# Performance work log

Hardware: AMD Instinct MI355X
Metric: run time of the kernel (lower is better)

Reference implementation:

```python
import math
import jax, jax.numpy as jnp
import numpy as np

SAMPLE_RATIO = 0.25
K_NN = 5


def grid_index(loc_orig, H, W):
    # loc in [-1,1] -> nearest grid cell index (row-major)
    loc = jnp.clip(loc_orig, -1.0, 1.0) * 0.5 + 0.5
    ix = jnp.clip(jnp.round(loc[..., 0] * (W - 1)).astype(jnp.int32), 0, W - 1)
    iy = jnp.clip(jnp.round(loc[..., 1] * (H - 1)).astype(jnp.int32), 0, H - 1)
    return iy * W + ix  # [B, N0]


def token2map(x, loc_orig, idx_agg, H, W):
    # scatter token features (replicated to original points) into HxW grid, cell-average
    B, N, C = x.shape
    N0 = idx_agg.shape[1]
    idx_hw = grid_index(loc_orig, H, W)
    off = jnp.arange(B, dtype=jnp.int32)[:, None]
    idx_hw_flat = (idx_hw + off * (H * W)).reshape(-1)
    value = jnp.ones((B * N0,), x.dtype)
    all_w = jax.ops.segment_sum(value, idx_hw_flat, num_segments=B * H * W) + 1e-6
    value = value / all_w[idx_hw_flat]
    x_src = jnp.take_along_axis(x, idx_agg[..., None], axis=1).reshape(B * N0, C)
    x_map = jax.ops.segment_sum(x_src * value[:, None], idx_hw_flat, num_segments=B * H * W)
    return x_map.reshape(B, H, W, C).transpose(0, 3, 1, 2)  # [B,C,H,W]


def map2token(x_map, N, loc_orig, idx_agg, agg_weight):
    # gather grid features back to tokens, weighted by per-token-normalized agg_weight
    B, C, H, W = x_map.shape
    N0 = idx_agg.shape[1]
    idx_hw = grid_index(loc_orig, H, W)
    off = jnp.arange(B, dtype=jnp.int32)[:, None]
    idx_tok_flat = (idx_agg + off * N).reshape(-1)
    idx_hw_flat = (idx_hw + off * (H * W)).reshape(-1)
    value = agg_weight.reshape(-1).astype(x_map.dtype)
    all_w = jax.ops.segment_sum(value, idx_tok_flat, num_segments=B * N) + 1e-6
    value = value / all_w[idx_tok_flat]
    feat = x_map.transpose(0, 2, 3, 1).reshape(B * H * W, C)[idx_hw_flat]
    out = jax.ops.segment_sum(feat * value[:, None], idx_tok_flat, num_segments=B * N)
    return out.reshape(B, N, C)


def cluster_dpc_knn(x, Ns, k):
    # DPC-KNN clustering (no_grad in original -> stop_gradient)
    B, N, C = x.shape
    x = jax.lax.stop_gradient(x)
    x2 = jnp.sum(x * x, axis=-1)
    d2 = x2[:, :, None] + x2[:, None, :] - 2.0 * jnp.einsum('bic,bjc->bij', x, x)
    dist = jnp.sqrt(jnp.maximum(d2, 0.0)) / jnp.sqrt(jnp.asarray(C, x.dtype))
    dist_nearest = -jax.lax.top_k(-dist, k)[0]                 # k smallest dists (incl self)
    density = jnp.exp(-jnp.mean(dist_nearest ** 2, axis=-1))    # [B,N]
    # deterministic tiny tie-break noise (original uses torch.rand*1e-6)
    density = density + jax.random.uniform(jax.random.key(42), density.shape, density.dtype) * 1e-6
    mask = (density[:, None, :] > density[:, :, None]).astype(x.dtype)
    dist_max = jnp.max(dist.reshape(B, -1), axis=-1)[:, None, None]
    dist_ind = jnp.min(dist * mask + dist_max * (1.0 - mask), axis=-1)
    score = dist_ind * density
    index_down = jax.lax.top_k(score, Ns)[1]                    # [B,Ns] cluster centers
    dist_c = jnp.take_along_axis(dist, index_down[:, :, None], axis=1)  # [B,Ns,N]
    idx_cluster = jnp.argmin(dist_c, axis=1).astype(jnp.int32)  # [B,N]
    # centers belong to their own cluster
    flat = (index_down + jnp.arange(B)[:, None] * N).reshape(-1)
    own = jnp.tile(jnp.arange(Ns, dtype=jnp.int32), B)
    idx_cluster = idx_cluster.reshape(-1).at[flat].set(own).reshape(B, N)
    return idx_cluster


def merge_tokens(x, idx_cluster, Ns, weight, idx_agg):
    # weighted average of tokens per cluster; propagate mapping/weights to original points
    B, N, C = x.shape
    idx = (idx_cluster + jnp.arange(B, dtype=jnp.int32)[:, None] * Ns).reshape(-1)
    w = weight.reshape(-1)
    all_w = jax.ops.segment_sum(w, idx, num_segments=B * Ns) + 1e-6
    nw = w / all_w[idx]
    x_merged = jax.ops.segment_sum(x.reshape(B * N, C) * nw[:, None], idx,
                                   num_segments=B * Ns).reshape(B, Ns, C)
    norm_weight = nw.reshape(B, N, 1)
    idx_agg_new = jnp.take_along_axis(idx_cluster, idx_agg, axis=1)          # [B,N0]
    weight_t = jnp.take_along_axis(norm_weight, idx_agg[..., None], axis=1)  # [B,N0,1]
    return x_merged, idx_agg_new, weight_t


def ctm_forward(x, loc_orig, idx_agg, agg_weight, conv_w, conv_b, skip_w, ln_g, ln_b,
                conf_w, conf_b, H, W):
    B, N, C = x.shape
    x_map = token2map(x, loc_orig, idx_agg, H, W)
    x_map = jax.lax.conv_general_dilated(
        x_map, conv_w, window_strides=(2, 2), padding=((1, 1), (1, 1)),
        dimension_numbers=('NCHW', 'OIHW', 'NCHW')) + conv_b[None, :, None, None]
    xt = map2token(x_map, N, loc_orig, idx_agg, agg_weight) + x @ skip_w.T
    mu = jnp.mean(xt, axis=-1, keepdims=True)
    var = jnp.mean((xt - mu) ** 2, axis=-1, keepdims=True)
    xt = (xt - mu) / jnp.sqrt(var + 1e-5) * ln_g + ln_b
    conf = xt @ conf_w.T + conf_b          # [B,N,1]
    weight = jnp.exp(conf)
    Ns = max(math.ceil(N * SAMPLE_RATIO), 1)
    idx_cluster = cluster_dpc_knn(xt, Ns, K_NN)
    x_down, idx_agg_down, weight_t = merge_tokens(xt, idx_cluster, Ns, weight, idx_agg)
    agg_weight_down = agg_weight * weight_t
    agg_weight_down = agg_weight_down / jnp.max(agg_weight_down, axis=1, keepdims=True)
    # down_block is identity in this reference
    return x_down, idx_agg_down, agg_weight_down


def setup_inputs() -> dict:
    key = jax.random.key(0)
    ks = jax.random.split(key, 10)
    B, N, C, C2, H, W = 4, 3136, 64, 128, 56, 56
    return {
        'x': jax.random.normal(ks[0], (B, N, C), jnp.float32),
        'loc_orig': jax.random.normal(ks[1], (B, N, 2), jnp.float32),
        'idx_agg': jax.random.randint(ks[2], (B, N), 0, N),
        'agg_weight': jax.random.uniform(ks[3], (B, N, 1), jnp.float32, 0.1, 1.0),
        'conv_w': jax.random.normal(ks[4], (C2, C, 3, 3), jnp.float32) * 0.02,
        'conv_b': jnp.zeros((C2,), jnp.float32),
        'skip_w': jax.random.normal(ks[5], (C2, C), jnp.float32) * 0.02,
        'ln_g': jnp.ones((C2,), jnp.float32),
        'ln_b': jnp.zeros((C2,), jnp.float32),
        'conf_w': jax.random.normal(ks[6], (1, C2), jnp.float32) * 0.02,
        'conf_b': jnp.zeros((1,), jnp.float32),
        'H': 56,
        'W': 56,
    }


def reference(x, loc_orig, idx_agg, agg_weight, conv_w, conv_b, skip_w, ln_g, ln_b,
              conf_w, conf_b, H, W):
    return ctm_forward(x, loc_orig, idx_agg, agg_weight, conv_w, conv_b, skip_w,
                       ln_g, ln_b, conf_w, conf_b, H, W)
```

## Files before the change

### kernel.cpp

```cpp
#include <hip/hip_runtime.h>
#include <math.h>
#include <float.h>

#define Bq   4
#define Nq   3136
#define Cq   64
#define C2q  128
#define Hq   56
#define Wq   56
#define HWq  (Hq*Wq)
#define HOq  28
#define WOq  28
#define HWOq (HOq*WOq)
#define NSq  784
#define KNN  5
#define BNq  (Bq*Nq)

#define T64   64
#define KC    32
#define NIT64 (Nq/T64)
#define NT_C  ((NSq+T64-1)/T64)
#define NSPL  8
#define NSPA  2
#define LDP   34

__device__ __constant__ int c_spl[NSPL + 1]  = {0, 7, 13, 19, 25, 31, 37, 43, 49};
__device__ __constant__ int c_spla[NSPA + 1] = {0, 7, 13};

typedef unsigned int   u32;
typedef unsigned long long u64;
typedef __attribute__((ext_vector_type(4))) double d64x4;

static __device__ __forceinline__ void atomicMaxPosD(double* p, double v) {
    atomicMax((u64*)p, (u64)__double_as_longlong(v));
}
static __device__ __forceinline__ int clampTok(int t) {
    return min(max(t, 0), Nq - 1);
}

static __device__ __forceinline__ void ins5(double* a, double v) {
    if (v < a[KNN - 1]) {
        a[KNN - 1] = v;
        #pragma unroll
        for (int m = KNN - 1; m > 0; m--)
            if (a[m] < a[m - 1]) { double t = a[m]; a[m] = a[m - 1]; a[m - 1] = t; }
    }
}
static __device__ __forceinline__ void cex(double& a, double& b) {
    double lo = fmin(a, b), hi = fmax(a, b); a = lo; b = hi;
}
static __device__ __forceinline__ void merge5(double* a, const double* p) {
    double t0 = fmin(a[0], p[4]);
    double t1 = fmin(a[1], p[3]);
    double t2 = fmin(a[2], p[2]);
    double t3 = fmin(a[3], p[1]);
    double t4 = fmin(a[4], p[0]);
    cex(t0, t1); cex(t1, t2); cex(t2, t3); cex(t3, t4);
    cex(t0, t1); cex(t1, t2); cex(t2, t3);
    cex(t0, t1); cex(t1, t2);
    cex(t0, t1);
    a[0] = t0; a[1] = t1; a[2] = t2; a[3] = t3; a[4] = t4;
}

static __device__ __forceinline__ int mfma_mode_probe(int l4, int l15) {
    d64x4 p;
    #pragma unroll
    for (int v = 0; v < 4; v++) p[v] = 0.0;
    double a1 = (l4 == 0) ? (double)(16 * l15) : 0.0;
    double b1 = (l4 == 0) ? 1.0 : 0.0;
    p = __builtin_amdgcn_mfma_f64_16x16x4f64(a1, b1, p, 0, 0, 0);
    double a2 = (l4 == 0) ? 1.0 : 0.0;
    double b2 = (l4 == 0) ? (double)l15 : 0.0;
    p = __builtin_amdgcn_mfma_f64_16x16x4f64(a2, b2, p, 0, 0, 0);
    bool ok0 = true, ok1 = true;
    #pragma unroll
    for (int v = 0; v < 4; v++) {
        ok0 = ok0 && (p[v] == (double)(16 * (4 * l4 + v) + l15));
        ok1 = ok1 && (p[v] == (double)(16 * (l4 + 4 * v) + l15));
    }
    return __all(ok0) ? 0 : (__all(ok1) ? 1 : 2);
}

static __device__ __forceinline__ u32 rotl32(u32 x, int d) { return (x << d) | (x >> (32 - d)); }
static __device__ __forceinline__ float tf_uniform(int t) {
    const u32 k0 = 0u, k1 = 42u;
    const u32 ks2 = k0 ^ k1 ^ 0x1BD11BDAu;
    u32 ks[3] = { k0, k1, ks2 };
    bool lo = (t < 6272);
    u32 cx0 = lo ? (u32)t : (u32)(t - 6272);
    u32 cx1 = lo ? (u32)(t + 6272) : (u32)t;
    u32 x0 = cx0 + ks[0];
// ... 70 lines not shown
              const float* __restrict__ bias, double* xmap28T) {
    __shared__ double sIn[2][9][Cq];
    int blk = blockIdx.x;
    int b  = blk & (Bq - 1);
    int cp = blk >> 2;
    int tid = threadIdx.x;
    int co = tid & (C2q - 1);
    int cl = tid >> 7;
    const double* xb = xmap56T + (size_t)b * HWq * Cq;
    for (int idx = tid; idx < 2 * 9 * Cq; idx += 256) {
        int cell_l = idx / (9 * Cq);
        int rem = idx - cell_l * (9 * Cq);
        int tap = rem >> 6;
        int ci  = rem & 63;
        int cell = 2 * cp + cell_l;
        int ox = cell % WOq, oy = cell / WOq;
        int ky = tap / 3, kx = tap - ky * 3;
        int iy = 2 * oy + ky - 1, ix = 2 * ox + kx - 1;
        double v = 0.0;
        if (iy >= 0 && iy < Hq && ix >= 0 && ix < Wq)
            v = xb[(size_t)(iy * Wq + ix) * Cq + ci];
        sIn[cell_l][tap][ci] = v;
    }
    __syncthreads();
    double acc = (double)bias[co];
    for (int ci = 0; ci < Cq; ci++) {
        #pragma unroll
        for (int tap = 0; tap < 9; tap++)
            acc += sIn[cl][tap][ci] * (double)wT[(size_t)(ci * 9 + tap) * C2q + co];
    }
    int cell = 2 * cp + cl;
    xmap28T[((size_t)b * HWOq + cell) * C2q + co] = acc;
}

__global__ void ctm_m2t(const double* __restrict__ xmap28T, const float* __restrict__ aggw,
                        const int* __restrict__ idx_agg, const int* __restrict__ cell28,
                        const double* __restrict__ allwtok, double* xt) {
    int id = blockIdx.x * blockDim.x + threadIdx.x;
    if (id >= BNq * C2q) return;
    int t = id / C2q, c = id - t * C2q;
    int b = t / Nq;
    int tok = clampTok(idx_agg[t]);
    double v = (double)aggw[t] / (allwtok[b * Nq + tok] + 1e-6);
    double f = xmap28T[((size_t)b * HWOq + cell28[t]) * C2q + c];
    atomicAdd(&xt[(size_t)(b * Nq + tok) * C2q + c], f * v);
}

__global__ __launch_bounds__(C2q)
void ctm_finalize(double* xt, const float* __restrict__ x, const float* __restrict__ skipw,
                  const float* __restrict__ lng, const float* __restrict__ lnb,
                  const float* __restrict__ confw, const float* __restrict__ confb,
                  double* x2o, double* weightv) {
    int bn = blockIdx.x; int c = threadIdx.x;
    double* row = xt + (size_t)bn * C2q;
    const float* xr = x + (size_t)bn * Cq;
    double acc = row[c];
    const float* sw = skipw + c * Cq;
    #pragma unroll 16
    for (int k = 0; k < Cq; k++) acc += (double)xr[k] * (double)sw[k];
    __shared__ double red[C2q];
    __shared__ double stat[2];
    red[c] = acc; __syncthreads();
    for (int off = C2q / 2; off > 0; off >>= 1) { if (c < off) red[c] += red[c + off]; __syncthreads(); }
    if (c == 0) stat[0] = red[0] * (1.0 / C2q);
    __syncthreads();
    double mu = stat[0];
    double d = acc - mu;
    red[c] = d * d; __syncthreads();
    for (int off = C2q / 2; off > 0; off >>= 1) { if (c < off) red[c] += red[c + off]; __syncthreads(); }
    if (c == 0) stat[1] = red[0] * (1.0 / C2q);
    __syncthreads();
    double var = stat[1];
    double v = d / sqrt(var + 1e-5) * (double)lng[c] + (double)lnb[c];
    row[c] = v;
    red[c] = v * v; __syncthreads();
    for (int off = C2q / 2; off > 0; off >>= 1) { if (c < off) red[c] += red[c + off]; __syncthreads(); }
    if (c == 0) x2o[bn] = red[0];
    __syncthreads();
    red[c] = v * (double)confw[c]; __syncthreads();
    for (int off = C2q / 2; off > 0; off >>= 1) { if (c < off) red[c] += red[c + off]; __syncthreads(); }
    if (c == 0) weightv[bn] = exp(red[0] + (double)confb[0]);
}


__global__ __launch_bounds__(256, 2)
void ctm_pass1(const double* __restrict__ xt, const double* __restrict__ x2,
               double* pbest, double* pmax) {
    __shared__ double sBB[2][T64][LDP];
    __shared__ double sx2j[2][T64];
    int blk = blockIdx.x;
    int b  = blk & (Bq - 1);
    int s  = (blk >> 2) & (NSPL - 1);
    int it = blk >> 5;
    int tid = threadIdx.x;
    const double* xtb = xt + (size_t)b * Nq * C2q;
    const double* x2b = x2 + (size_t)b * Nq;
    int i0 = it * T64;
    int jt_beg = c_spl[s], jt_end = c_spl[s + 1];

    int wv = tid >> 6, ln = tid & 63;
    int l15 = ln & 15, l4 = ln >> 4;
    int mode = mfma_mode_probe(l4, l15);

    if (mode < 2) {
        int rw[4];
        #pragma unroll
        for (int v = 0; v < 4; v++) rw[v] = (mode == 0) ? (4 * l4 + v) : (l4 + 4 * v);
        int rbase = i0 + wv * 16;
        double a_reg[4][8];
        const double* arow = xtb + (size_t)(i0 + wv * 16 + l15) * C2q + l4;
        #pragma unroll
        for (int kc = 0; kc < 4; kc++)
            #pragma unroll
            for (int st = 0; st < 8; st++)
                a_reg[kc][st] = arow[kc * KC + 4 * st];
        double x2i[4];
        #pragma unroll
        for (int v = 0; v < 4; v++) x2i[v] = x2b[rbase + rw[v]];
        double best[4][KNN]; double mx[4];
        #pragma unroll
        for (int v = 0; v < 4; v++) {
            mx[v] = -DBL_MAX;
            #pragma unroll
            for (int k = 0; k < KNN; k++) best[v][k] = DBL_MAX;
        }
        {
            int j0 = jt_beg * T64;
            #pragma unroll
            for (int w = 0; w < 4; w++) {
                int idx = tid + w * 256; int r = idx >> 4, c = (idx & 15) * 2;
                *(double2*)&sBB[0][r][c] = *(const double2*)&xtb[(size_t)(j0 + r) * C2q + c];
            }
            if (tid < T64) sx2j[0][tid] = x2b[j0 + tid];
        }
        __syncthreads();
        int q = 0;
        for (int jt = jt_beg; jt < jt_end; jt++) {
            int j0 = jt * T64;
            d64x4 acc[4];
            #pragma unroll
            for (int bc = 0; bc < 4; bc++)
                #pragma unroll
                for (int v = 0; v < 4; v++) acc[bc][v] = 0.0;
            #pragma unroll
            for (int kc = 0; kc < 4; kc++) {
                const int cb = kc & 1, nb = cb ^ 1, nkc = (kc + 1) & 3;
                const bool lastk = (kc == 3);
                bool hn = !lastk || (jt + 1 < jt_end);
                int nj0 = lastk ? j0 + T64 : j0;
                double2 sreg[4]; double xr = 0.0;
                if (hn) {
                    #pragma unroll
                    for (int w = 0; w < 4; w++) {
                        int idx = tid + w * 256; int r = idx >> 4, c = (idx & 15) * 2;
                        sreg[w] = *(const double2*)&xtb[(size_t)(nj0 + r) * C2q + nkc * KC + c];
                    }
                    if (lastk && tid < T64) xr = x2b[nj0 + tid];
                }
                #pragma unroll
                for (int st = 0; st < 8; st++) {
                    double av = a_reg[kc][st];
                    #pragma unroll
                    for (int bc = 0; bc < 4; bc++) {
                        double bv = sBB[cb][bc * 16 + l15][4 * st + l4];
                        acc[bc] = __builtin_amdgcn_mfma_f64_16x16x4f64(av, bv, acc[bc], 0, 0, 0);
                    }
                }
                if (hn) {
                    #pragma unroll
                    for (int w = 0; w < 4; w++) {
                        int idx = tid + w * 256; int r = idx >> 4, c = (idx & 15) * 2;
                        *(double2*)&sBB[nb][r][c] = sreg[w];
                    }
                    if (lastk && tid < T64) sx2j[q ^ 1][tid] = xr;
                }
                __syncthreads();
            }
            #pragma unroll
            for (int bc = 0; bc < 4; bc++) {
                double xj = sx2j[q][bc * 16 + l15];
                #pragma unroll
                for (int v = 0; v < 4; v++) {
                    double d2 = x2i[v] + xj - 2.0 * acc[bc][v];
                    mx[v] = fmax(mx[v], d2);
                    ins5(best[v], d2);
                }
            }
            q ^= 1;
        }
        for (int m = 1; m <= 8; m <<= 1) {
            #pragma unroll
            for (int v = 0; v < 4; v++) {
                double p[KNN];
                #pragma unroll
                for (int k = 0; k < KNN; k++) p[k] = __shfl_xor(best[v][k], m);
                mx[v] = fmax(mx[v], __shfl_xor(mx[v], m));
                merge5(best[v], p);
            }
        }
        if (l15 == 0) {
            #pragma unroll
            for (int v = 0; v < 4; v++) {
                int gi = b * Nq + rbase + rw[v];
                size_t base = ((size_t)s * BNq + gi) * KNN;
                #pragma unroll
                for (int k = 0; k < KNN; k++) pbest[base + k] = best[v][k];
                pmax[(size_t)s * BNq + gi] = mx[v];
            }
        }
    } else {
        double (*sA)[LDP] = sBB[0];
        double (*sB)[LDP] = sBB[1];
        int tx = tid & 15, ty = tid >> 4;
        double x2i[4];
        #pragma unroll
        for (int r = 0; r < 4; r++) x2i[r] = x2b[i0 + ty + 16 * r];
        double best[4][KNN]; double mx[4];
        #pragma unroll
        for (int r = 0; r < 4; r++) {
            mx[r] = -DBL_MAX;
            #pragma unroll
            for (int k = 0; k < KNN; k++) best[r][k] = DBL_MAX;
        }
        for (int jt = jt_beg; jt < jt_end; jt++) {
            int j0 = jt * T64;
            double acc[4][4];
            #pragma unroll
            for (int r = 0; r < 4; r++)
                #pragma unroll
                for (int q = 0; q < 4; q++) acc[r][q] = 0.0;
            for (int kc = 0; kc < 4; kc++) {
                __syncthreads();
                #pragma unroll
                for (int idx = tid; idx < T64 * KC / 2; idx += 256) {
                    int r = idx >> 4, c = (idx & 15) * 2;
                    *(double2*)&sA[r][c] = *(const double2*)&xtb[(size_t)(i0 + r) * C2q + kc * KC + c];
                    *(double2*)&sB[r][c] = *(const double2*)&xtb[(size_t)(j0 + r) * C2q + kc * KC + c];
                }
                if (kc == 0 && tid < T64) sx2j[0][tid] = x2b[j0 + tid];
                __syncthreads();
                #pragma unroll 4
                for (int cc = 0; cc < KC; cc += 2) {
                    double2 xi[4], xj[4];
                    #pragma unroll
                    for (int r = 0; r < 4; r++) xi[r] = *(const double2*)&sA[ty + 16 * r][cc];
                    #pragma unroll
                    for (int q = 0; q < 4; q++) xj[q] = *(const double2*)&sB[tx + 16 * q][cc];
                    #pragma unroll
                    for (int r = 0; r < 4; r++)
                        #pragma unroll
                        for (int q = 0; q < 4; q++) acc[r][q] += xi[r].x * xj[q].x;
                    #pragma unroll
                    for (int r = 0; r < 4; r++)
                        #pragma unroll
                        for (int q = 0; q < 4; q++) acc[r][q] += xi[r].y * xj[q].y;
                }
            }
            #pragma unroll
            for (int r = 0; r < 4; r++)
                #pragma unroll
                for (int q = 0; q < 4; q++) {
                    double d2 = x2i[r] + sx2j[0][tx + 16 * q] - 2.0 * acc[r][q];
                    mx[r] = fmax(mx[r], d2);
                    ins5(best[r], d2);
                }
        }
        for (int m = 1; m <= 8; m <<= 1) {
            #pragma unroll
            for (int r = 0; r < 4; r++) {
                double p[KNN];
                #pragma unroll
                for (int k = 0; k < KNN; k++) p[k] = __shfl_xor(best[r][k], m);
                mx[r] = fmax(mx[r], __shfl_xor(mx[r], m));
                merge5(best[r], p);
            }
        }
        if (tx == 0) {
            #pragma unroll
            for (int r = 0; r < 4; r++) {
                int gi = b * Nq + i0 + ty + 16 * r;
                size_t base = ((size_t)s * BNq + gi) * KNN;
                #pragma unroll
                for (int k = 0; k < KNN; k++) pbest[base + k] = best[r][k];
                pmax[(size_t)s * BNq + gi] = mx[r];
            }
        }
    }
}

__global__ void ctm_merge1(const double* __restrict__ pbest, const double* __restrict__ pmax,
                           double* density, double* maxd2) {
    int t = blockIdx.x * blockDim.x + threadIdx.x;
    if (t >= BNq) return;
    double a[KNN];
    #pragma unroll
    for (int k = 0; k < KNN; k++) a[k] = pbest[(size_t)t * KNN + k];
    double mxv = pmax[t];
    #pragma unroll
    for (int s = 1; s < NSPL; s++) {
        double p[KNN];
        #pragma unroll
        for (int k = 0; k < KNN; k++) p[k] = pbest[((size_t)s * BNq + t) * KNN + k];
        merge5(a, p);
        mxv = fmax(mxv, pmax[(size_t)s * BNq + t]);
    }
    double sum = 0.0;
    #pragma unroll
    for (int k = 0; k < KNN; k++) sum += fmax(a[k], 0.0);
    density[t] = exp(-sum / (double)(C2q * KNN)) + (double)(tf_uniform(t) * 1e-6f);
    atomicMaxPosD(&maxd2[t / Nq], mxv);
}

__global__ __launch_bounds__(256, 2)
void ctm_pass2(const double* __restrict__ xt, const double* __restrict__ x2,
               const double* __restrict__ density, double* pmin) {
    __shared__ double sBB[2][T64][LDP];
    __shared__ double sx2j[2][T64];
    __shared__ double sdj[2][T64];
    int blk = blockIdx.x;
    int b  = blk & (Bq - 1);
    int s  = (blk >> 2) & (NSPL - 1);
    int it = blk >> 5;
    int tid = threadIdx.x;
    const double* xtb = xt + (size_t)b * Nq * C2q;
    const double* x2b = x2 + (size_t)b * Nq;
    const double* db  = density + (size_t)b * Nq;
    int i0 = it * T64;
    int jt_beg = c_spl[s], jt_end = c_spl[s + 1];

    int wv = tid >> 6, ln = tid & 63;
    int l15 = ln & 15, l4 = ln >> 4;
    int mode = mfma_mode_probe(l4, l15);

    if (mode < 2) {
        int rw[4];
        #pragma unroll
        for (int v = 0; v < 4; v++) rw[v] = (mode == 0) ? (4 * l4 + v) : (l4 + 4 * v);
        int rbase = i0 + wv * 16;
        double a_reg[4][8];
        const double* arow = xtb + (size_t)(i0 + wv * 16 + l15) * C2q + l4;
        #pragma unroll
        for (int kc = 0; kc < 4; kc++)
            #pragma unroll
            for (int st = 0; st < 8; st++)
                a_reg[kc][st] = arow[kc * KC + 4 * st];
        double x2i[4], di[4], mn[4];
        #pragma unroll
        for (int v = 0; v < 4; v++) {
            x2i[v] = x2b[rbase + rw[v]];
            di[v]  = db[rbase + rw[v]];
            mn[v]  = DBL_MAX;
        }
        {
            int j0 = jt_beg * T64;
            #pragma unroll
            for (int w = 0; w < 4; w++) {
                int idx = tid + w * 256; int r = idx >> 4, c = (idx & 15) * 2;
                *(double2*)&sBB[0][r][c] = *(const double2*)&xtb[(size_t)(j0 + r) * C2q + c];
            }
            if (tid < T64) { sx2j[0][tid] = x2b[j0 + tid]; sdj[0][tid] = db[j0 + tid]; }
        }
        __syncthreads();
        int q = 0;
        for (int jt = jt_beg; jt < jt_end; jt++) {
            int j0 = jt * T64;
            d64x4 acc[4];
            #pragma unroll
            for (int bc = 0; bc < 4; bc++)
                #pragma unroll
                for (int v = 0; v < 4; v++) acc[bc][v] = 0.0;
            #pragma unroll
            for (int kc = 0; kc < 4; kc++) {
                const int cb = kc & 1, nb = cb ^ 1, nkc = (kc + 1) & 3;
                const bool lastk = (kc == 3);
                bool hn = !lastk || (jt + 1 < jt_end);
                int nj0 = lastk ? j0 + T64 : j0;
                double2 sreg[4]; double xr = 0.0, dr = 0.0;
                if (hn) {
                    #pragma unroll
                    for (int w = 0; w < 4; w++) {
                        int idx = tid + w * 256; int r = idx >> 4, c = (idx & 15) * 2;
                        sreg[w] = *(const double2*)&xtb[(size_t)(nj0 + r) * C2q + nkc * KC + c];
                    }
                    if (lastk && tid < T64) { xr = x2b[nj0 + tid]; dr = db[nj0 + tid]; }
                }
                #pragma unroll
                for (int st = 0; st < 8; st++) {
                    double av = a_reg[kc][st];
                    #pragma unroll
                    for (int bc = 0; bc < 4; bc++) {
                        double bv = sBB[cb][bc * 16 + l15][4 * st + l4];
                        acc[bc] = __builtin_amdgcn_mfma_f64_16x16x4f64(av, bv, acc[bc], 0, 0, 0);
                    }
                }
                if (hn) {
                    #pragma unroll
                    for (int w = 0; w < 4; w++) {
                        int idx = tid + w * 256; int r = idx >> 4, c = (idx & 15) * 2;
                        *(double2*)&sBB[nb][r][c] = sreg[w];
                    }
                    if (lastk && tid < T64) { sx2j[q ^ 1][tid] = xr; sdj[q ^ 1][tid] = dr; }
                }
                __syncthreads();
            }
            #pragma unroll
            for (int bc = 0; bc < 4; bc++) {
                double xj = sx2j[q][bc * 16 + l15];
                double dj = sdj[q][bc * 16 + l15];
                #pragma unroll
                for (int v = 0; v < 4; v++) {
                    double d2 = x2i[v] + xj - 2.0 * acc[bc][v];
                    if (dj > di[v]) mn[v] = fmin(mn[v], d2);
                }
            }
            q ^= 1;
        }
        for (int m = 1; m <= 8; m <<= 1) {
            #pragma unroll
            for (int v = 0; v < 4; v++) mn[v] = fmin(mn[v], __shfl_xor(mn[v], m));
        }
        if (l15 == 0) {
            #pragma unroll
            for (int v = 0; v < 4; v++) {
                int gi = b * Nq + rbase + rw[v];
                pmin[(size_t)s * BNq + gi] = mn[v];
            }
        }
    } else {
        double (*sA)[LDP] = sBB[0];
        double (*sB)[LDP] = sBB[1];
        int tx = tid & 15, ty = tid >> 4;
        double x2i[4], di[4], mn[4];
        #pragma unroll
        for (int r = 0; r < 4; r++) {
            x2i[r] = x2b[i0 + ty + 16 * r];
            di[r]  = db[i0 + ty + 16 * r];
            mn[r]  = DBL_MAX;
        }
        for (int jt = jt_beg; jt < jt_end; jt++) {
            int j0 = jt * T64;
            double acc[4][4];
            #pragma unroll
            for (int r = 0; r < 4; r++)
                #pragma unroll
                for (int q = 0; q < 4; q++) acc[r][q] = 0.0;
            for (int kc = 0; kc < 4; kc++) {
                __syncthreads();
                #pragma unroll
                for (int idx = tid; idx < T64 * KC / 2; idx += 256) {
                    int r = idx >> 4, c = (idx & 15) * 2;
                    *(double2*)&sA[r][c] = *(const double2*)&xtb[(size_t)(i0 + r) * C2q + kc * KC + c];
                    *(double2*)&sB[r][c] = *(const double2*)&xtb[(size_t)(j0 + r) * C2q + kc * KC + c];
                }
                if (kc == 0 && tid < T64) { sx2j[0][tid] = x2b[j0 + tid]; sdj[0][tid] = db[j0 + tid]; }
                __syncthreads();
                #pragma unroll 4
                for (int cc = 0; cc < KC; cc += 2) {
                    double2 xi[4], xj[4];
                    #pragma unroll
                    for (int r = 0; r < 4; r++) xi[r] = *(const double2*)&sA[ty + 16 * r][cc];
                    #pragma unroll
                    for (int q = 0; q < 4; q++) xj[q] = *(const double2*)&sB[tx + 16 * q][cc];
                    #pragma unroll
                    for (int r = 0; r < 4; r++)
                        #pragma unroll
                        for (int q = 0; q < 4; q++) acc[r][q] += xi[r].x * xj[q].x;
                    #pragma unroll
                    for (int r = 0; r < 4; r++)
                        #pragma unroll
                        for (int q = 0; q < 4; q++) acc[r][q] += xi[r].y * xj[q].y;
                }
            }
            #pragma unroll
            for (int r = 0; r < 4; r++)
                #pragma unroll
                for (int q = 0; q < 4; q++) {
                    double d2 = x2i[r] + sx2j[0][tx + 16 * q] - 2.0 * acc[r][q];
                    if (sdj[0][tx + 16 * q] > di[r]) mn[r] = fmin(mn[r], d2);
                }
        }
        for (int m = 1; m <= 8; m <<= 1) {
            #pragma unroll
            for (int r = 0; r < 4; r++) mn[r] = fmin(mn[r], __shfl_xor(mn[r], m));
        }
        if (tx == 0) {
            #pragma unroll
            for (int r = 0; r < 4; r++) {
                int gi = b * Nq + i0 + ty + 16 * r;
                pmin[(size_t)s * BNq + gi] = mn[r];
            }
        }
    }
}

__global__ void ctm_merge2(const double* __restrict__ pmin, const double* __restrict__ maxd2,
                           const double* __restrict__ density, double* score) {
    int t = blockIdx.x * blockDim.x + threadIdx.x;
    if (t >= BNq) return;
    int b = t / Nq;
    double m = pmin[t];
    #pragma unroll
    for (int s = 1; s < NSPL; s++) m = fmin(m, pmin[(size_t)s * BNq + t]);
    double mm = fmin(maxd2[b], m);
    score[t] = sqrt(fmax(mm, 0.0)) / sqrt((double)C2q) * density[t];
}

__global__ __launch_bounds__(1024)
void ctm_sort(const double* __restrict__ score, int* index_down) {
    __shared__ double s[4096];
    __shared__ int   si[4096];
    int b = blockIdx.x, tid = threadIdx.x;
    for (int i = tid; i < 4096; i += 1024) {
        if (i < Nq) {
            double v = score[b * Nq + i];
            s[i] = isnan(v) ? -DBL_MAX : v;
            si[i] = i;
        } else { s[i] = -DBL_MAX; si[i] = 0x7fffffff; }
    }
    __syncthreads();
    for (int k = 2; k <= 4096; k <<= 1) {
        for (int j = k >> 1; j > 0; j >>= 1) {
            for (int i = tid; i < 4096; i += 1024) {
                int ixj = i ^ j;
                if (ixj > i) {
                    double s1 = s[i], s2 = s[ixj];
                    int i1 = si[i], i2 = si[ixj];
                    bool before_ij = (s1 > s2) || (s1 == s2 && i1 < i2);
                    bool before_ji = (s2 > s1) || (s2 == s1 && i2 < i1);
                    bool doswap = ((i & k) == 0) ? before_ji : before_ij;
                    if (doswap) { s[i] = s2; s[ixj] = s1; si[i] = i2; si[ixj] = i1; }
                }
            }
            __syncthreads();
        }
    }
    for (int t = tid; t < NSq; t += 1024) {
        int v = si[t];
        index_down[b * NSq + t] = ((unsigned)v < (unsigned)Nq) ? v : 0;
    }
}

__global__ __launch_bounds__(256, 2)
void ctm_assign(const double* __restrict__ xt, const double* __restrict__ x2,
                const int* __restrict__ index_down, double* pbd, int* pbs) {
    __shared__ double sBB[2][T64][LDP];
    __shared__ double sx2c[T64];
    __shared__ int    sidx[T64];
    int blk = blockIdx.x;
    int b  = blk & (Bq - 1);
    int s  = (blk >> 2) & (NSPA - 1);
    int it = blk >> 3;
    int tid = threadIdx.x;
    const double* xtb = xt + (size_t)b * Nq * C2q;
    const double* x2b = x2 + (size_t)b * Nq;
    int i0 = it * T64;
    int jt_beg = c_spla[s], jt_end = c_spla[s + 1];

// ... 218 lines not shown
}

__global__ void ctm_out2(const double* __restrict__ awd, const double* __restrict__ maxawd, float* out2) {
    int t = blockIdx.x * blockDim.x + threadIdx.x;
    if (t >= BNq) return;
    int b = t / Nq;
    out2[t] = (float)(awd[t] / maxawd[b]);
}

extern "C" void kernel_launch(void* const* d_in, const int* in_sizes, int n_in,
                              void* d_out, int out_size, void* d_ws, size_t ws_size,
                              hipStream_t stream) {
    const float* x     = (const float*)d_in[0];
    const float* loc   = (const float*)d_in[1];
    const int*   idxag = (const int*)  d_in[2];
    const float* aggw  = (const float*)d_in[3];
    const float* convw = (const float*)d_in[4];
    const float* convb = (const float*)d_in[5];
    const float* skipw = (const float*)d_in[6];
    const float* lng   = (const float*)d_in[7];
    const float* lnb   = (const float*)d_in[8];
    const float* confw = (const float*)d_in[9];
    const float* confb = (const float*)d_in[10];
    (void)in_sizes; (void)n_in;

    char* w = (char*)d_ws;
    size_t off = 0;
    auto alloc = [&](size_t bytes) -> void* {
        void* p = w + off; off = (off + bytes + 255) & ~(size_t)255; return p;
    };

    int*    cnt56   = (int*)   alloc((size_t)BNq * 4);
    double* allwtok = (double*)alloc((size_t)BNq * 8);
    double* xt      = (double*)alloc((size_t)BNq * C2q * 8);
    double* arena   = (double*)alloc((size_t)Bq * HWq * Cq * 8);
    double* allwc   = (double*)alloc((size_t)Bq * NSq * 8);
    double* maxawd  = (double*)alloc((size_t)Bq * 8);
    double* maxd2   = (double*)alloc((size_t)Bq * 8);
    size_t zero_bytes = off;
    int*    cell56   = (int*)   alloc((size_t)BNq * 4);
    int*    cell28   = (int*)   alloc((size_t)BNq * 4);
    double* xmap28T  = (double*)alloc((size_t)Bq * HWOq * C2q * 8);
    float*  wT       = (float*) alloc((size_t)C2q * Cq * 9 * 4);
    double* x2       = (double*)alloc((size_t)BNq * 8);
    double* density  = (double*)alloc((size_t)BNq * 8);
    double* score    = (double*)alloc((size_t)BNq * 8);
    int*    indexdn  = (int*)   alloc((size_t)Bq * NSq * 4);
    int*    idxclu   = (int*)   alloc((size_t)BNq * 4);
    double* nw       = (double*)alloc((size_t)BNq * 8);
    double* weightv  = (double*)alloc((size_t)BNq * 8);
    double* awd      = (double*)alloc((size_t)BNq * 8);
    double* pbest    = (double*)alloc((size_t)NSPL * BNq * KNN * 8);
    double* pmax     = (double*)alloc((size_t)NSPL * BNq * 8);
    double* pmin     = (double*)alloc((size_t)NSPL * BNq * 8);
    double* pbd      = (double*)alloc((size_t)NSPA * BNq * 8);
    int*    pbs      = (int*)   alloc((size_t)NSPA * BNq * 4);
    size_t required = off;

    const int tb = 256;
    float* out = (float*)d_out;

    if (ws_size < required) {
        ctm_fallback<<<(out_size + tb - 1) / tb, tb, 0, stream>>>(out, out_size);
        return;
    }

    double* xmap56T = arena;
    double* xmerged = arena;

    hipMemsetAsync(d_ws, 0, zero_bytes, stream);

    ctm_prep<<<(BNq + tb - 1) / tb, tb, 0, stream>>>(loc, idxag, aggw, cell56, cell28, cnt56, allwtok);
    ctm_wt<<<((C2q * Cq * 9) + tb - 1) / tb, tb, 0, stream>>>(convw, wT);
    ctm_t2m<<<((BNq * Cq) + tb - 1) / tb, tb, 0, stream>>>(x, idxag, cell56, cnt56, xmap56T);
    ctm_conv<<<Bq * (HWOq / 2), 256, 0, stream>>>(xmap56T, wT, convb, xmap28T);
    ctm_m2t<<<((BNq * C2q) + tb - 1) / tb, tb, 0, stream>>>(xmap28T, aggw, idxag, cell28, allwtok, xt);
    ctm_finalize<<<BNq, C2q, 0, stream>>>(xt, x, skipw, lng, lnb, confw, confb, x2, weightv);
    ctm_pass1<<<Bq * NSPL * NIT64, 256, 0, stream>>>(xt, x2, pbest, pmax);
    ctm_merge1<<<(BNq + tb - 1) / tb, tb, 0, stream>>>(pbest, pmax, density, maxd2);
    ctm_pass2<<<Bq * NSPL * NIT64, 256, 0, stream>>>(xt, x2, density, pmin);
    ctm_merge2<<<(BNq + tb - 1) / tb, tb, 0, stream>>>(pmin, maxd2, density, score);
    ctm_sort<<<Bq, 1024, 0, stream>>>(score, indexdn);
    ctm_assign<<<Bq * NSPA * NIT64, 256, 0, stream>>>(xt, x2, indexdn, pbd, pbs);
    ctm_merge3<<<(BNq + tb - 1) / tb, tb, 0, stream>>>(pbd, pbs, idxclu);
    ctm_override<<<((Bq * NSq) + tb - 1) / tb, tb, 0, stream>>>(indexdn, idxclu);
    ctm_zeromerged<<<((Bq * NSq * C2q) + tb - 1) / tb, tb, 0, stream>>>(xmerged);
    ctm_merge_w<<<(BNq + tb - 1) / tb, tb, 0, stream>>>(idxclu, weightv, allwc);
    ctm_merge_x<<<((BNq * C2q) + tb - 1) / tb, tb, 0, stream>>>(idxclu, weightv, allwc, xt, nw, xmerged);

    ctm_out0<<<((Bq * NSq * C2q) + tb - 1) / tb, tb, 0, stream>>>(xmerged, out);
    ctm_out12<<<(BNq + tb - 1) / tb, tb, 0, stream>>>(idxag, idxclu, nw, aggw,
                                                      out + (size_t)Bq * NSq * C2q, awd, maxawd);
    ctm_out2<<<(BNq + tb - 1) / tb, tb, 0, stream>>>(awd, maxawd,
                                                     out + (size_t)Bq * NSq * C2q + BNq);
}
```

Before: 1.237 ms.

## Cache pairwise distances in pass1 and replace pass2 GEMM with streaming min scan

New measurement: 1.237 ms. About the same (+0.0%).

```diff
diff --git a/kernel.cpp b/kernel.cpp
--- a/kernel.cpp
+++ b/kernel.cpp
@@ -213,40 +213,48 @@
                   const float* __restrict__ confw, const float* __restrict__ confb,
                   double* x2o, double* weightv) {
     int bn = blockIdx.x; int c = threadIdx.x;
+    int lane = c & 63, w = c >> 6;
     double* row = xt + (size_t)bn * C2q;
     const float* xr = x + (size_t)bn * Cq;
     double acc = row[c];
     const float* sw = skipw + c * Cq;
     #pragma unroll 16
     for (int k = 0; k < Cq; k++) acc += (double)xr[k] * (double)sw[k];
-    __shared__ double red[C2q];
-    __shared__ double stat[2];
-    red[c] = acc; __syncthreads();
-    for (int off = C2q / 2; off > 0; off >>= 1) { if (c < off) red[c] += red[c + off]; __syncthreads(); }
-    if (c == 0) stat[0] = red[0] * (1.0 / C2q);
+    __shared__ double slot[4][2];
+    double s = acc;
+    #pragma unroll
+    for (int m = 1; m <= 32; m <<= 1) s += __shfl_xor(s, m);
+    if (lane == 0) slot[0][w] = s;
     __syncthreads();
-    double mu = stat[0];
+    double mu = (slot[0][0] + slot[0][1]) * (1.0 / C2q);
     double d = acc - mu;
-    red[c] = d * d; __syncthreads();
-    for (int off = C2q / 2; off > 0; off >>= 1) { if (c < off) red[c] += red[c + off]; __syncthreads(); }
-    if (c == 0) stat[1] = red[0] * (1.0 / C2q);
+    s = d * d;
+    #pragma unroll
+    for (int m = 1; m <= 32; m <<= 1) s += __shfl_xor(s, m);
+    if (lane == 0) slot[1][w] = s;
     __syncthreads();
-    double var = stat[1];
+    double var = (slot[1][0] + slot[1][1]) * (1.0 / C2q);
     double v = d / sqrt(var + 1e-5) * (double)lng[c] + (double)lnb[c];
     row[c] = v;
-    red[c] = v * v; __syncthreads();
-    for (int off = C2q / 2; off > 0; off >>= 1) { if (c < off) red[c] += red[c + off]; __syncthreads(); }
-    if (c == 0) x2o[bn] = red[0];
+    s = v * v;
+    #pragma unroll
+    for (int m = 1; m <= 32; m <<= 1) s += __shfl_xor(s, m);
+    if (lane == 0) slot[2][w] = s;
+    double s2 = v * (double)confw[c];
+    #pragma unroll
+    for (int m = 1; m <= 32; m <<= 1) s2 += __shfl_xor(s2, m);
+    if (lane == 0) slot[3][w] = s2;
     __syncthreads();
-    red[c] = v * (double)confw[c]; __syncthreads();
-    for (int off = C2q / 2; off > 0; off >>= 1) { if (c < off) red[c] += red[c + off]; __syncthreads(); }
-    if (c == 0) weightv[bn] = exp(red[0] + (double)confb[0]);
+    if (c == 0) {
+        x2o[bn] = slot[2][0] + slot[2][1];
+        weightv[bn] = exp(slot[3][0] + slot[3][1] + (double)confb[0]);
+    }
 }
 
 
 __global__ __launch_bounds__(256, 2)
 void ctm_pass1(const double* __restrict__ xt, const double* __restrict__ x2,
-               double* pbest, double* pmax) {
+               double* pbest, double* pmax, double* d2buf, int dostore) {
     __shared__ double sBB[2][T64][LDP];
     __shared__ double sx2j[2][T64];
     int blk = blockIdx.x;
@@ -343,6 +351,8 @@
                 #pragma unroll
                 for (int v = 0; v < 4; v++) {
                     double d2 = x2i[v] + xj - 2.0 * acc[bc][v];
+                    if (dostore)
+                        d2buf[(size_t)(b * Nq + rbase + rw[v]) * Nq + (j0 + bc * 16 + l15)] = d2;
                     mx[v] = fmax(mx[v], d2);
                     ins5(best[v], d2);
                 }
@@ -422,6 +432,8 @@
                 #pragma unroll
                 for (int q = 0; q < 4; q++) {
                     double d2 = x2i[r] + sx2j[0][tx + 16 * q] - 2.0 * acc[r][q];
+                    if (dostore)
+                        d2buf[(size_t)(b * Nq + i0 + ty + 16 * r) * Nq + (j0 + tx + 16 * q)] = d2;
                     mx[r] = fmax(mx[r], d2);
                     ins5(best[r], d2);
                 }
@@ -470,6 +482,36 @@
     for (int k = 0; k < KNN; k++) sum += fmax(a[k], 0.0);
     density[t] = exp(-sum / (double)(C2q * KNN)) + (double)(tf_uniform(t) * 1e-6f);
     atomicMaxPosD(&maxd2[t / Nq], mxv);
+}
+
+__global__ __launch_bounds__(256)
+void ctm_pass2s(const double* __restrict__ d2buf, const double* __restrict__ density,
+                double* pmin2) {
+    int gid = blockIdx.x * 4 + (threadIdx.x >> 6);
+    int lane = threadIdx.x & 63;
+    if (gid >= BNq) return;
+    int b = gid / Nq;
+    int i = gid - b * Nq;
+    const double* dr = d2buf + (size_t)gid * Nq;
+    const double* db = density + (size_t)b * Nq;
+    double di = db[i];
+    double mn = DBL_MAX;
+    for (int j = lane; j < Nq; j += 64) {
+        double d2 = dr[j];
+        if (db[j] > di) mn = fmin(mn, d2);
+    }
+    #pragma unroll
+    for (int m = 1; m <= 32; m <<= 1) mn = fmin(mn, __shfl_xor(mn, m));
+    if (lane == 0) pmin2[gid] = mn;
+}
+
+__global__ void ctm_merge2s(const double* __restrict__ pmin2, const double* __restrict__ maxd2,
+                            const double* __restrict__ density, double* score) {
+    int t = blockIdx.x * blockDim.x + threadIdx.x;
+    if (t >= BNq) return;
+    int b = t / Nq;
+    double mm = fmin(maxd2[b], pmin2[t]);
+    score[t] = sqrt(fmax(mm, 0.0)) / sqrt((double)C2q) * density[t];
 }
 
 __global__ __launch_bounds__(256, 2)
@@ -992,6 +1034,8 @@
     double* pbd      = (double*)alloc((size_t)NSPA * BNq * 8);
     int*    pbs      = (int*)   alloc((size_t)NSPA * BNq * 4);
     size_t required = off;
+    double* d2buf    = (double*)alloc((size_t)BNq * Nq * 8);
+    size_t required_fast = off;
 
     const int tb = 256;
     float* out = (float*)d_out;
@@ -1000,6 +1044,7 @@
         ctm_fallback<<<(out_size + tb - 1) / tb, tb, 0, stream>>>(out, out_size);
         return;
     }
+    const bool fast = (ws_size >= required_fast);
 
     double* xmap56T = arena;
     double* xmerged = arena;
@@ -1012,10 +1057,15 @@
     ctm_conv<<<Bq * (HWOq / 2), 256, 0, stream>>>(xmap56T, wT, convb, xmap28T);
     ctm_m2t<<<((BNq * C2q) + tb - 1) / tb, tb, 0, stream>>>(xmap28T, aggw, idxag, cell28, allwtok, xt);
     ctm_finalize<<<BNq, C2q, 0, stream>>>(xt, x, skipw, lng, lnb, confw, confb, x2, weightv);
-    ctm_pass1<<<Bq * NSPL * NIT64, 256, 0, stream>>>(xt, x2, pbest, pmax);
+    ctm_pass1<<<Bq * NSPL * NIT64, 256, 0, stream>>>(xt, x2, pbest, pmax, d2buf, fast ? 1 : 0);
     ctm_merge1<<<(BNq + tb - 1) / tb, tb, 0, stream>>>(pbest, pmax, density, maxd2);
-    ctm_pass2<<<Bq * NSPL * NIT64, 256, 0, stream>>>(xt, x2, density, pmin);
-    ctm_merge2<<<(BNq + tb - 1) / tb, tb, 0, stream>>>(pmin, maxd2, density, score);
+    if (fast) {
+        ctm_pass2s<<<(BNq + 3) / 4, 256, 0, stream>>>(d2buf, density, pmin);
+        ctm_merge2s<<<(BNq + tb - 1) / tb, tb, 0, stream>>>(pmin, maxd2, density, score);
+    } else {
+        ctm_pass2<<<Bq * NSPL * NIT64, 256, 0, stream>>>(xt, x2, density, pmin);
+        ctm_merge2<<<(BNq + tb - 1) / tb, tb, 0, stream>>>(pmin, maxd2, density, score);
+    }
     ctm_sort<<<Bq, 1024, 0, stream>>>(score, indexdn);
     ctm_assign<<<Bq * NSPA * NIT64, 256, 0, stream>>>(xt, x2, indexdn, pbd, pbs);
     ctm_merge3<<<(BNq + tb - 1) / tb, tb, 0, stream>>>(pbd, pbs, idxclu);
```

## Sort tokens by density and compute only lower-triangular tiles for parent distance

Applied to the files above, without the earlier changes.

Result: no change. 1.218 ms (-1.5%).

```diff
diff --git a/kernel.cpp b/kernel.cpp
--- a/kernel.cpp
+++ b/kernel.cpp
@@ -19,7 +19,7 @@
 #define T64   64
 #define KC    32
 #define NIT64 (Nq/T64)
-#define NT_C  ((NSq+T64-1)/T64)
+#define NPAIR (NIT64*(NIT64+1)/2)
 #define NSPL  8
 #define NSPA  2
 #define LDP   34
@@ -37,6 +37,16 @@
 static __device__ __forceinline__ int clampTok(int t) {
     return min(max(t, 0), Nq - 1);
 }
+
+static __device__ __forceinline__ u64 encD(double d) {
+    u64 u = (u64)__double_as_longlong(d);
+    return (u >> 63) ? ~u : (u | 0x8000000000000000ULL);
+}
+static __device__ __forceinline__ double decD(u64 u) {
+    u64 o = (u >> 63) ? (u ^ 0x8000000000000000ULL) : ~u;
+    return __longlong_as_double((long long)o);
+}
+#define ENC_DBL_MAX 0xFFEFFFFFFFFFFFFFULL
 
 static __device__ __forceinline__ void ins5(double* a, double v) {
     if (v < a[KNN - 1]) {
@@ -213,34 +223,42 @@
                   const float* __restrict__ confw, const float* __restrict__ confb,
                   double* x2o, double* weightv) {
     int bn = blockIdx.x; int c = threadIdx.x;
+    int lane = c & 63, w = c >> 6;
     double* row = xt + (size_t)bn * C2q;
     const float* xr = x + (size_t)bn * Cq;
     double acc = row[c];
     const float* sw = skipw + c * Cq;
     #pragma unroll 16
     for (int k = 0; k < Cq; k++) acc += (double)xr[k] * (double)sw[k];
-    __shared__ double red[C2q];
-    __shared__ double stat[2];
-    red[c] = acc; __syncthreads();
-    for (int off = C2q / 2; off > 0; off >>= 1) { if (c < off) red[c] += red[c + off]; __syncthreads(); }
-    if (c == 0) stat[0] = red[0] * (1.0 / C2q);
+    __shared__ double slot[4][2];
+    double s = acc;
+    #pragma unroll
+    for (int m = 1; m <= 32; m <<= 1) s += __shfl_xor(s, m);
+    if (lane == 0) slot[0][w] = s;
     __syncthreads();
-    double mu = stat[0];
+    double mu = (slot[0][0] + slot[0][1]) * (1.0 / C2q);
     double d = acc - mu;
-    red[c] = d * d; __syncthreads();
-    for (int off = C2q / 2; off > 0; off >>= 1) { if (c < off) red[c] += red[c + off]; __syncthreads(); }
-    if (c == 0) stat[1] = red[0] * (1.0 / C2q);
+    s = d * d;
+    #pragma unroll
+    for (int m = 1; m <= 32; m <<= 1) s += __shfl_xor(s, m);
+    if (lane == 0) slot[1][w] = s;
     __syncthreads();
-    double var = stat[1];
+    double var = (slot[1][0] + slot[1][1]) * (1.0 / C2q);
     double v = d / sqrt(var + 1e-5) * (double)lng[c] + (double)lnb[c];
     row[c] = v;
-    red[c] = v * v; __syncthreads();
-    for (int off = C2q / 2; off > 0; off >>= 1) { if (c < off) red[c] += red[c + off]; __syncthreads(); }
-    if (c == 0) x2o[bn] = red[0];
+    s = v * v;
+    #pragma unroll
+    for (int m = 1; m <= 32; m <<= 1) s += __shfl_xor(s, m);
+    if (lane == 0) slot[2][w] = s;
+    double s2 = v * (double)confw[c];
+    #pragma unroll
+    for (int m = 1; m <= 32; m <<= 1) s2 += __shfl_xor(s2, m);
+    if (lane == 0) slot[3][w] = s2;
     __syncthreads();
-    red[c] = v * (double)confw[c]; __syncthreads();
-    for (int off = C2q / 2; off > 0; off >>= 1) { if (c < off) red[c] += red[c + off]; __syncthreads(); }
-    if (c == 0) weightv[bn] = exp(red[0] + (double)confb[0]);
+    if (c == 0) {
+        x2o[bn] = slot[2][0] + slot[2][1];
+        weightv[bn] = exp(slot[3][0] + slot[3][1] + (double)confb[0]);
+    }
 }
 
 
@@ -472,23 +490,72 @@
     atomicMaxPosD(&maxd2[t / Nq], mxv);
 }
 
+__global__ __launch_bounds__(1024)
+void ctm_sortd(const double* __restrict__ density, int* perm) {
+    __shared__ double s[4096];
+    __shared__ int   si[4096];
+    int b = blockIdx.x, tid = threadIdx.x;
+    for (int i = tid; i < 4096; i += 1024) {
+        if (i < Nq) {
+            double v = density[b * Nq + i];
+            s[i] = isnan(v) ? -DBL_MAX : v;
+            si[i] = i;
+        } else { s[i] = -DBL_MAX; si[i] = 0x7fffffff; }
+    }
+    __syncthreads();
+    for (int k = 2; k <= 4096; k <<= 1) {
+        for (int j = k >> 1; j > 0; j >>= 1) {
+            for (int i = tid; i < 4096; i += 1024) {
+                int ixj = i ^ j;
+                if (ixj > i) {
+                    double s1 = s[i], s2 = s[ixj];
+                    int i1 = si[i], i2 = si[ixj];
+                    bool before_ij = (s1 > s2) || (s1 == s2 && i1 < i2);
+                    bool before_ji = (s2 > s1) || (s2 == s1 && i2 < i1);
+                    bool doswap = ((i & k) == 0) ? before_ji : before_ij;
+                    if (doswap) { s[i] = s2; s[ixj] = s1; si[i] = i2; si[ixj] = i1; }
+                }
+            }
+            __syncthreads();
+        }
+    }
+    for (int t = tid; t < Nq; t += 1024) {
+        int v = si[t];
+        perm[b * Nq + t] = ((unsigned)v < (unsigned)Nq) ? v : 0;
+    }
+}
+
+__global__ void ctm_initmin(u64* pmin2u) {
+    int t = blockIdx.x * blockDim.x + threadIdx.x;
+    if (t < BNq) pmin2u[t] = ENC_DBL_MAX;
+}
+
 __global__ __launch_bounds__(256, 2)
-void ctm_pass2(const double* __restrict__ xt, const double* __restrict__ x2,
-               const double* __restrict__ density, double* pmin) {
+void ctm_pass2t(const double* __restrict__ xt, const double* __restrict__ x2,
+                const double* __restrict__ density, const int* __restrict__ perm,
+                u64* pmin2u) {
     __shared__ double sBB[2][T64][LDP];
-    __shared__ double sx2j[2][T64];
-    __shared__ double sdj[2][T64];
+    __shared__ double sx2j[T64];
+    __shared__ double sdj[T64];
+    __shared__ int    sI[T64];
+    __shared__ int    sJ[T64];
+    __shared__ double sp[4][T64];
     int blk = blockIdx.x;
-    int b  = blk & (Bq - 1);
-    int s  = (blk >> 2) & (NSPL - 1);
-    int it = blk >> 5;
+    int b = blk & (Bq - 1);
+    int p = blk >> 2;
+    int it = (int)((sqrt(8.0 * (double)p + 1.0) - 1.0) * 0.5);
+    while ((it + 1) * (it + 2) / 2 <= p) ++it;
+    while (it * (it + 1) / 2 > p) --it;
+    int jt = p - it * (it + 1) / 2;
+    int i0 = it * T64, j0 = jt * T64;
     int tid = threadIdx.x;
     const double* xtb = xt + (size_t)b * Nq * C2q;
     const double* x2b = x2 + (size_t)b * Nq;
     const double* db  = density + (size_t)b * Nq;
-    int i0 = it * T64;
-    int jt_beg = c_spl[s], jt_end = c_spl[s + 1];
-
+    const int* pb = perm + b * Nq;
+    if (tid < T64) sI[tid] = pb[i0 + tid];
+    else if (tid < 2 * T64) sJ[tid - T64] = pb[j0 + tid - T64];
+    __syncthreads();
     int wv = tid >> 6, ln = tid & 63;
     int l15 = ln & 15, l4 = ln >> 4;
     int mode = mfma_mode_probe(l4, l15);
@@ -497,84 +564,75 @@
         int rw[4];
         #pragma unroll
         for (int v = 0; v < 4; v++) rw[v] = (mode == 0) ? (4 * l4 + v) : (l4 + 4 * v);
-        int rbase = i0 + wv * 16;
+        int rloc = wv * 16;
         double a_reg[4][8];
-        const double* arow = xtb + (size_t)(i0 + wv * 16 + l15) * C2q + l4;
+        const double* arow = xtb + (size_t)sI[rloc + l15] * C2q + l4;
         #pragma unroll
         for (int kc = 0; kc < 4; kc++)
             #pragma unroll
             for (int st = 0; st < 8; st++)
                 a_reg[kc][st] = arow[kc * KC + 4 * st];
-        double x2i[4], di[4], mn[4];
+        double x2i[4], di[4];
         #pragma unroll
         for (int v = 0; v < 4; v++) {
-            x2i[v] = x2b[rbase + rw[v]];
-            di[v]  = db[rbase + rw[v]];
-            mn[v]  = DBL_MAX;
-        }
-        {
-            int j0 = jt_beg * T64;
-            #pragma unroll
-            for (int w = 0; w < 4; w++) {
-                int idx = tid + w * 256; int r = idx >> 4, c = (idx & 15) * 2;
-                *(double2*)&sBB[0][r][c] = *(const double2*)&xtb[(size_t)(j0 + r) * C2q + c];
-            }
-            if (tid < T64) { sx2j[0][tid] = x2b[j0 + tid]; sdj[0][tid] = db[j0 + tid]; }
-        }
+            int o = sI[rloc + rw[v]];
+            x2i[v] = x2b[o];
+            di[v]  = db[o];
+        }
+        #pragma unroll
+        for (int w = 0; w < 4; w++) {
+            int idx = tid + w * 256; int r = idx >> 4, c = (idx & 15) * 2;
+            *(double2*)&sBB[0][r][c] = *(const double2*)&xtb[(size_t)sJ[r] * C2q + c];
+        }
+        if (tid < T64) { int o = sJ[tid]; sx2j[tid] = x2b[o]; sdj[tid] = db[o]; }
         __syncthreads();
-        int q = 0;
-        for (int jt = jt_beg; jt < jt_end; jt++) {
-            int j0 = jt * T64;
-            d64x4 acc[4];
-            #pragma unroll
-            for (int bc = 0; bc < 4; bc++)
-                #pragma unroll
-                for (int v = 0; v < 4; v++) acc[bc][v] = 0.0;
-            #pragma unroll
-            for (int kc = 0; kc < 4; kc++) {
-                const int cb = kc & 1, nb = cb ^ 1, nkc = (kc + 1) & 3;
-                const bool lastk = (kc == 3);
-                bool hn = !lastk || (jt + 1 < jt_end);
-                int nj0 = lastk ? j0 + T64 : j0;
-                double2 sreg[4]; double xr = 0.0, dr = 0.0;
-                if (hn) {
-                    #pragma unroll
-                    for (int w = 0; w < 4; w++) {
-                        int idx = tid + w * 256; int r = idx >> 4, c = (idx & 15) * 2;
-                        sreg[w] = *(const double2*)&xtb[(size_t)(nj0 + r) * C2q + nkc * KC + c];
-                    }
-                    if (lastk && tid < T64) { xr = x2b[nj0 + tid]; dr = db[nj0 + tid]; }
-                }
-                #pragma unroll
-                for (int st = 0; st < 8; st++) {
-                    double av = a_reg[kc][st];
-                    #pragma unroll
-                    for (int bc = 0; bc < 4; bc++) {
-                        double bv = sBB[cb][bc * 16 + l15][4 * st + l4];
-                        acc[bc] = __builtin_amdgcn_mfma_f64_16x16x4f64(av, bv, acc[bc], 0, 0, 0);
-                    }
-                }
-                if (hn) {
-                    #pragma unroll
-                    for (int w = 0; w < 4; w++) {
-                        int idx = tid + w * 256; int r = idx >> 4, c = (idx & 15) * 2;
-                        *(double2*)&sBB[nb][r][c] = sreg[w];
-                    }
-                    if (lastk && tid < T64) { sx2j[q ^ 1][tid] = xr; sdj[q ^ 1][tid] = dr; }
-                }
-                __syncthreads();
-            }
-            #pragma unroll
-            for (int bc = 0; bc < 4; bc++) {
-                double xj = sx2j[q][bc * 16 + l15];
-                double dj = sdj[q][bc * 16 + l15];
-                #pragma unroll
-                for (int v = 0; v < 4; v++) {
-                    double d2 = x2i[v] + xj - 2.0 * acc[bc][v];
-                    if (dj > di[v]) mn[v] = fmin(mn[v], d2);
-                }
-            }
-            q ^= 1;
+        d64x4 acc[4];
+        #pragma unroll
+        for (int bc = 0; bc < 4; bc++)
+            #pragma unroll
+            for (int v = 0; v < 4; v++) acc[bc][v] = 0.0;
+        #pragma unroll
+        for (int kc = 0; kc < 4; kc++) {
+            const int cb = kc & 1, nb = cb ^ 1;
+            const bool hn = (kc < 3);
+            double2 sreg[4];
+            if (hn) {
+                #pragma unroll
+                for (int w = 0; w < 4; w++) {
+                    int idx = tid + w * 256; int r = idx >> 4, c = (idx & 15) * 2;
+                    sreg[w] = *(const double2*)&xtb[(size_t)sJ[r] * C2q + (kc + 1) * KC + c];
+                }
+            }
+            #pragma unroll
+            for (int st = 0; st < 8; st++) {
+                double av = a_reg[kc][st];
+                #pragma unroll
+                for (int bc = 0; bc < 4; bc++) {
+                    double bv = sBB[cb][bc * 16 + l15][4 * st + l4];
+                    acc[bc] = __builtin_amdgcn_mfma_f64_16x16x4f64(av, bv, acc[bc], 0, 0, 0);
+                }
+            }
+            if (hn) {
+                #pragma unroll
+                for (int w = 0; w < 4; w++) {
+                    int idx = tid + w * 256; int r = idx >> 4, c = (idx & 15) * 2;
+                    *(double2*)&sBB[nb][r][c] = sreg[w];
+                }
+            }
+            __syncthreads();
+        }
+        double mn[4];
+        #pragma unroll
+        for (int v = 0; v < 4; v++) mn[v] = DBL_MAX;
+        #pragma unroll
+        for (int bc = 0; bc < 4; bc++) {
+            double xj = sx2j[bc * 16 + l15];
+            double dj = sdj[bc * 16 + l15];
+            #pragma unroll
+            for (int v = 0; v < 4; v++) {
+                double d2 = x2i[v] + xj - 2.0 * acc[bc][v];
+                if (dj > di[v]) mn[v] = fmin(mn[v], d2);
+            }
         }
         for (int m = 1; m <= 8; m <<= 1) {
             #pragma unroll
@@ -582,88 +640,47 @@
         }
         if (l15 == 0) {
             #pragma unroll
-            for (int v = 0; v < 4; v++) {
-                int gi = b * Nq + rbase + rw[v];
-                pmin[(size_t)s * BNq + gi] = mn[v];
-            }
+            for (int v = 0; v < 4; v++)
+                if (mn[v] < DBL_MAX)
+                    atomicMin(&pmin2u[b * Nq + i0 + rloc + rw[v]], encD(mn[v]));
         }
     } else {
-        double (*sA)[LDP] = sBB[0];
-        double (*sB)[LDP] = sBB[1];
-        int tx = tid & 15, ty = tid >> 4;
-        double x2i[4], di[4], mn[4];
-        #pragma unroll
-        for (int r = 0; r < 4; r++) {
-            x2i[r] = x2b[i0 + ty + 16 * r];
-            di[r]  = db[i0 + ty + 16 * r];
-            mn[r]  = DBL_MAX;
-        }
-        for (int jt = jt_beg; jt < jt_end; jt++) {
-            int j0 = jt * T64;
-            double acc[4][4];
-            #pragma unroll
-            for (int r = 0; r < 4; r++)
-                #pragma unroll
-                for (int q = 0; q < 4; q++) acc[r][q] = 0.0;
-            for (int kc = 0; kc < 4; kc++) {
-                __syncthreads();
-                #pragma unroll
-                for (int idx = tid; idx < T64 * KC / 2; idx += 256) {
-                    int r = idx >> 4, c = (idx & 15) * 2;
-                    *(double2*)&sA[r][c] = *(const double2*)&xtb[(size_t)(i0 + r) * C2q + kc * KC + c];
-                    *(double2*)&sB[r][c] = *(const double2*)&xtb[(size_t)(j0 + r) * C2q + kc * KC + c];
-                }
-                if (kc == 0 && tid < T64) { sx2j[0][tid] = x2b[j0 + tid]; sdj[0][tid] = db[j0 + tid]; }
-                __syncthreads();
-                #pragma unroll 4
-                for (int cc = 0; cc < KC; cc += 2) {
-                    double2 xi[4], xj[4];
-                    #pragma unroll
-                    for (int r = 0; r < 4; r++) xi[r] = *(const double2*)&sA[ty + 16 * r][cc];
-                    #pragma unroll
-                    for (int q = 0; q < 4; q++) xj[q] = *(const double2*)&sB[tx + 16 * q][cc];
-                    #pragma unroll
-                    for (int r = 0; r < 4; r++)
-                        #pragma unroll
-                        for (int q = 0; q < 4; q++) acc[r][q] += xi[r].x * xj[q].x;
-                    #pragma unroll
-                    for (int r = 0; r < 4; r++)
-                        #pragma unroll
-                        for (int q = 0; q < 4; q++) acc[r][q] += xi[r].y * xj[q].y;
-                }
-            }
-            #pragma unroll
-            for (int r = 0; r < 4; r++)
-                #pragma unroll
-                for (int q = 0; q < 4; q++) {
-                    double d2 = x2i[r] + sx2j[0][tx + 16 * q] - 2.0 * acc[r][q];
-                    if (sdj[0][tx + 16 * q] > di[r]) mn[r] = fmin(mn[r], d2);
-                }
-        }
-        for (int m = 1; m <= 8; m <<= 1) {
-            #pragma unroll
-            for (int r = 0; r < 4; r++) mn[r] = fmin(mn[r], __shfl_xor(mn[r], m));
-        }
-        if (tx == 0) {
-            #pragma unroll
-            for (int r = 0; r < 4; r++) {
-                int gi = b * Nq + i0 + ty + 16 * r;
-                pmin[(size_t)s * BNq + gi] = mn[r];
-            }
-        }
-    }
-}
-
-__global__ void ctm_merge2(const double* __restrict__ pmin, const double* __restrict__ maxd2,
-                           const double* __restrict__ density, double* score) {
+        int rl = tid & 63;
+        int cg = tid >> 6;
+        int ro = sI[rl];
+        double x2i = x2b[ro];
+        double di = db[ro];
+        const double* xr = xtb + (size_t)ro * C2q;
+        double mn = DBL_MAX;
+        for (int cc = 0; cc < 16; cc++) {
+            int co = sJ[cg * 16 + cc];
+            if (db[co] > di) {
+                const double* xc = xtb + (size_t)co * C2q;
+                double dot = 0.0;
+                for (int k = 0; k < C2q; k++) dot += xr[k] * xc[k];
+                mn = fmin(mn, x2i + x2b[co] - 2.0 * dot);
+            }
+        }
+        sp[cg][rl] = mn;
+        __syncthreads();
+        if (cg == 0) {
+            mn = fmin(fmin(sp[0][rl], sp[1][rl]), fmin(sp[2][rl], sp[3][rl]));
+            if (mn < DBL_MAX)
+                atomicMin(&pmin2u[b * Nq + i0 + rl], encD(mn));
+        }
+    }
+}
+
+__global__ void ctm_merge2t(const u64* __restrict__ pmin2u, const double* __restrict__ maxd2,
+                            const double* __restrict__ density, const int* __restrict__ perm,
+                            double* score) {
     int t = blockIdx.x * blockDim.x + threadIdx.x;
     if (t >= BNq) return;
     int b = t / Nq;
-    double m = pmin[t];
-    #pragma unroll
-    for (int s = 1; s < NSPL; s++) m = fmin(m, pmin[(size_t)s * BNq + t]);
+    double m = decD(pmin2u[t]);
     double mm = fmin(maxd2[b], m);
-    score[t] = sqrt(fmax(mm, 0.0)) / sqrt((double)C2q) * density[t];
+    int orig = b * Nq + perm[t];
+    score[orig] = sqrt(fmax(mm, 0.0)) / sqrt((double)C2q) * density[orig];
 }
 
 __global__ __launch_bounds__(1024)
@@ -988,10 +1005,12 @@
     double* awd      = (double*)alloc((size_t)BNq * 8);
     double* pbest    = (double*)alloc((size_t)NSPL * BNq * KNN * 8);
     double* pmax     = (double*)alloc((size_t)NSPL * BNq * 8);
-    double* pmin     = (double*)alloc((size_t)NSPL * BNq * 8);
     double* pbd      = (double*)alloc((size_t)NSPA * BNq * 8);
     int*    pbs      = (int*)   alloc((size_t)NSPA * BNq * 4);
     size_t required = off;
+
+    int* perm   = (int*)pbest;
+    u64* pmin2u = (u64*)((char*)pbest + 131072);
 
     const int tb = 256;
     float* out = (float*)d_out;
@@ -1014,8 +1033,10 @@
     ctm_finalize<<<BNq, C2q, 0, stream>>>(xt, x, skipw, lng, lnb, confw, confb, x2, weightv);
     ctm_pass1<<<Bq * NSPL * NIT64, 256, 0, stream>>>(xt, x2, pbest, pmax);
     ctm_merge1<<<(BNq + tb - 1) / tb, tb, 0, stream>>>(pbest, pmax, density, maxd2);
-    ctm_pass2<<<Bq * NSPL * NIT64, 256, 0, stream>>>(xt, x2, density, pmin);
-    ctm_merge2<<<(BNq + tb - 1) / tb, tb, 0, stream>>>(pmin, maxd2, density, score);
+    ctm_sortd<<<Bq, 1024, 0, stream>>>(density, perm);
+    ctm_initmin<<<(BNq + tb - 1) / tb, tb, 0, stream>>>(pmin2u);
+    ctm_pass2t<<<Bq * NPAIR, 256, 0, stream>>>(xt, x2, density, perm, pmin2u);
+    ctm_merge2t<<<(BNq + tb - 1) / tb, tb, 0, stream>>>(pmin2u, maxd2, density, perm, score);
     ctm_sort<<<Bq, 1024, 0, stream>>>(score, indexdn);
     ctm_assign<<<Bq * NSPA * NIT64, 256, 0, stream>>>(xt, x2, indexdn, pbd, pbs);
     ctm_merge3<<<(BNq + tb - 1) / tb, tb, 0, stream>>>(pbd, pbs, idxclu);
```
